# Performance work log

Measured on AMD Instinct MI355X. Metric: run time of the kernel, lower is better.

## Reference

```python
import jax, jax.numpy as jnp
import numpy as np

B, S, D, H = 8, 2048, 1024, 4
HD = D // H


def _layernorm(x, w, b, eps=1e-5):
    mu = jnp.mean(x, axis=-1, keepdims=True)
    var = jnp.mean((x - mu) ** 2, axis=-1, keepdims=True)
    return (x - mu) * jax.lax.rsqrt(var + eps) * w + b


def setup_inputs() -> dict:
    key = jax.random.key(0)
    ks = jax.random.split(key, 10)
    s = 1.0 / np.sqrt(D)
    return {
        "text_representation": jax.random.normal(ks[0], (B, S, D), jnp.float32),
        "image_representation": jax.random.normal(ks[1], (B, S, D), jnp.float32),
        "ln_t_w": jnp.ones((D,), jnp.float32),
        "ln_t_b": jnp.zeros((D,), jnp.float32),
        "ln_i_w": jnp.ones((D,), jnp.float32),
        "ln_i_b": jnp.zeros((D,), jnp.float32),
        "Wa": jax.random.uniform(ks[2], (H, HD, D), jnp.float32, -s, s),
        "Wa_b": jax.random.uniform(ks[3], (H, HD), jnp.float32, -s, s),
        "Wq": jax.random.uniform(ks[4], (H, HD, D), jnp.float32, -s, s),
        "Wq_b": jax.random.uniform(ks[5], (H, HD), jnp.float32, -s, s),
        "sim_w": jax.random.uniform(ks[6], (HD, 1), jnp.float32, -1.0, 1.0),
        "sim_b": jax.random.uniform(ks[7], (HD,), jnp.float32, -1.0, 1.0),
        "fc_w": jax.random.uniform(ks[8], (1, H * HD), jnp.float32, -s, s),
        "fc_b": jax.random.uniform(ks[9], (1,), jnp.float32, -s, s),
    }


def reference(text_representation, image_representation, ln_t_w, ln_t_b,
              ln_i_w, ln_i_b, Wa, Wa_b, Wq, Wq_b, sim_w, sim_b, fc_w, fc_b):
    eps_cos = 1e-6
    text_rep = _layernorm(text_representation, ln_t_w, ln_t_b)   # [B,S,D]
    image_rep = _layernorm(image_representation, ln_i_w, ln_i_b)  # [B,S,D]
    # cosine similarity along last dim (torch-style norm clamping)
    tn = jnp.maximum(jnp.linalg.norm(text_rep, axis=-1), eps_cos)
    im = jnp.maximum(jnp.linalg.norm(image_rep, axis=-1), eps_cos)
    per_pos_sim = jnp.sum(text_rep * image_rep, axis=-1) / (tn * im)  # [B,S]
    global_sim = jnp.mean(per_pos_sim, axis=1, keepdims=True)          # [B,1]
    text_global = jnp.mean(text_rep, axis=1)    # [B,D]
    image_global = jnp.mean(image_rep, axis=1)  # [B,D]
    gate_a = jnp.einsum('bd,hkd->bhk', text_global, Wa) + Wa_b    # [B,H,HD]
    gate_q = jnp.einsum('bd,hkd->bhk', image_global, Wq) + Wq_b   # [B,H,HD]
    sim_feat = global_sim * sim_w[:, 0] + sim_b                   # [B,HD]
    gates = jax.nn.relu(gate_a + gate_q + sim_feat[:, None, :])   # [B,H,HD]
    combined = gates.reshape(gates.shape[0], H * HD)              # [B,H*HD]
    final_gate = jax.nn.sigmoid(combined @ fc_w.T + fc_b)         # [B,1]
    g = final_gate[:, :, None]                                    # [B,1,1]
    return g * text_rep + (1.0 - g) * image_rep
```

## Files before the change

kernel.cpp:

```cpp
#include <hip/hip_runtime.h>
#include <math.h>

#define BB 8
#define SS 2048
#define DD 1024
#define HH 4
#define HDD 256
#define NROW (BB*SS)
#define G 8
#define NSLICE (NROW/G)

#define OFF_MU_T 0
#define OFF_RS_T NROW
#define OFF_MU_I (2*NROW)
#define OFF_RS_I (3*NROW)
#define OFF_PT   (4*NROW)
#define OFF_PI   (OFF_PT + NSLICE*DD)
#define OFF_PS   (OFF_PI + NSLICE*DD)
#define OFF_TG   (OFF_PS + NSLICE)
#define OFF_IG   (OFF_TG + BB*DD)
#define OFF_SIM  (OFF_IG + BB*DD)
#define OFF_LOGIT (OFF_SIM + BB)

__device__ __forceinline__ float wred(float v) {
#pragma unroll
  for (int m = 32; m > 0; m >>= 1) v += __shfl_xor(v, m, 64);
  return v;
}

__device__ __forceinline__ float hsum(const float4 v) { return v.x+v.y+v.z+v.w; }
__device__ __forceinline__ float hsq(const float4 v)  { return v.x*v.x+v.y*v.y+v.z*v.z+v.w*v.w; }
__device__ __forceinline__ float hdot(const float4 a, const float4 b) {
  return a.x*b.x + a.y*b.y + a.z*b.z + a.w*b.w;
}

__global__ __launch_bounds__(256) void k1_stats(
    const float* __restrict__ text, const float* __restrict__ image,
    const float* __restrict__ wt, const float* __restrict__ bt,
    const float* __restrict__ wi, const float* __restrict__ bi,
    float* __restrict__ ws)
{
  const int g    = blockIdx.x;
  const int tid  = threadIdx.x;
  const int lane = tid & 63;
  const int wv   = tid >> 6;
  const int d0   = tid << 2;
  const int row0 = g * G;

  __shared__ float red1[4][8];
  __shared__ float red2[4][6];

  const float4 wt4 = *(const float4*)(wt + d0);
  const float4 bt4 = *(const float4*)(bt + d0);
  const float4 wi4 = *(const float4*)(wi + d0);
  const float4 bi4 = *(const float4*)(bi + d0);

  float4 tga = make_float4(0.f,0.f,0.f,0.f);
  float4 iga = make_float4(0.f,0.f,0.f,0.f);
  float sim_loc = 0.f;

  for (int r = 0; r < G; r += 2) {
    const size_t base0 = (size_t)(row0 + r) * DD + d0;
    const size_t base1 = base0 + DD;
    const float4 t0 = *(const float4*)(text  + base0);
    const float4 i0 = *(const float4*)(image + base0);
    const float4 t1 = *(const float4*)(text  + base1);
    const float4 i1 = *(const float4*)(image + base1);

    float a0 = hsum(t0), a1 = hsq(t0), a2 = hsum(i0), a3 = hsq(i0);
    float a4 = hsum(t1), a5 = hsq(t1), a6 = hsum(i1), a7 = hsq(i1);
    a0 = wred(a0); a1 = wred(a1); a2 = wred(a2); a3 = wred(a3);
    a4 = wred(a4); a5 = wred(a5); a6 = wred(a6); a7 = wred(a7);
    if (lane == 0) {
      red1[wv][0]=a0; red1[wv][1]=a1; red1[wv][2]=a2; red1[wv][3]=a3;
      red1[wv][4]=a4; red1[wv][5]=a5; red1[wv][6]=a6; red1[wv][7]=a7;
    }
    __syncthreads();
    float s[8];
#pragma unroll
    for (int q = 0; q < 8; ++q) s[q] = red1[0][q]+red1[1][q]+red1[2][q]+red1[3][q];
    const float invD = 1.f/DD;
    const float mt0 = s[0]*invD, rt0 = rsqrtf(s[1]*invD - mt0*mt0 + 1e-5f);
    const float mi0 = s[2]*invD, ri0 = rsqrtf(s[3]*invD - mi0*mi0 + 1e-5f);
    const float mt1 = s[4]*invD, rt1 = rsqrtf(s[5]*invD - mt1*mt1 + 1e-5f);
    const float mi1 = s[6]*invD, ri1 = rsqrtf(s[7]*invD - mi1*mi1 + 1e-5f);
    if (tid == 0) {
      const int row = row0 + r;
      ws[OFF_MU_T+row]=mt0;   ws[OFF_RS_T+row]=rt0;
      ws[OFF_MU_I+row]=mi0;   ws[OFF_RS_I+row]=ri0;
      ws[OFF_MU_T+row+1]=mt1; ws[OFF_RS_T+row+1]=rt1;
      ws[OFF_MU_I+row+1]=mi1; ws[OFF_RS_I+row+1]=ri1;
    }
    float4 tn0, in0, tn1, in1;
    tn0.x = (t0.x-mt0)*rt0*wt4.x + bt4.x;  tn0.y = (t0.y-mt0)*rt0*wt4.y + bt4.y;
    tn0.z = (t0.z-mt0)*rt0*wt4.z + bt4.z;  tn0.w = (t0.w-mt0)*rt0*wt4.w + bt4.w;
    in0.x = (i0.x-mi0)*ri0*wi4.x + bi4.x;  in0.y = (i0.y-mi0)*ri0*wi4.y + bi4.y;
    in0.z = (i0.z-mi0)*ri0*wi4.z + bi4.z;  in0.w = (i0.w-mi0)*ri0*wi4.w + bi4.w;
    tn1.x = (t1.x-mt1)*rt1*wt4.x + bt4.x;  tn1.y = (t1.y-mt1)*rt1*wt4.y + bt4.y;
    tn1.z = (t1.z-mt1)*rt1*wt4.z + bt4.z;  tn1.w = (t1.w-mt1)*rt1*wt4.w + bt4.w;
    in1.x = (i1.x-mi1)*ri1*wi4.x + bi4.x;  in1.y = (i1.y-mi1)*ri1*wi4.y + bi4.y;
    in1.z = (i1.z-mi1)*ri1*wi4.z + bi4.z;  in1.w = (i1.w-mi1)*ri1*wi4.w + bi4.w;

    tga.x += tn0.x + tn1.x; tga.y += tn0.y + tn1.y;
    tga.z += tn0.z + tn1.z; tga.w += tn0.w + tn1.w;
    iga.x += in0.x + in1.x; iga.y += in0.y + in1.y;
    iga.z += in0.z + in1.z; iga.w += in0.w + in1.w;

    float b0 = hdot(tn0,in0), b1 = hsq(tn0), b2 = hsq(in0);
    float b3 = hdot(tn1,in1), b4 = hsq(tn1), b5 = hsq(in1);
    b0 = wred(b0); b1 = wred(b1); b2 = wred(b2);
    b3 = wred(b3); b4 = wred(b4); b5 = wred(b5);
    if (lane == 0) {
      red2[wv][0]=b0; red2[wv][1]=b1; red2[wv][2]=b2;
      red2[wv][3]=b3; red2[wv][4]=b4; red2[wv][5]=b5;
    }
    __syncthreads();
    if (tid == 0) {
      float u[6];
#pragma unroll
      for (int q = 0; q < 6; ++q) u[q] = red2[0][q]+red2[1][q]+red2[2][q]+red2[3][q];
      sim_loc += u[0] / (fmaxf(sqrtf(u[1]),1e-6f) * fmaxf(sqrtf(u[2]),1e-6f));
      sim_loc += u[3] / (fmaxf(sqrtf(u[4]),1e-6f) * fmaxf(sqrtf(u[5]),1e-6f));
    }
  }
  *(float4*)(ws + OFF_PT + (size_t)g*DD + d0) = tga;
  *(float4*)(ws + OFF_PI + (size_t)g*DD + d0) = iga;
  if (tid == 0) ws[OFF_PS + g] = sim_loc;
}

__global__ __launch_bounds__(256) void kR_reduce(float* __restrict__ ws)
{
  const int tid = threadIdx.x;
  if (blockIdx.x < 256) {
    const int b   = blockIdx.x >> 5;
    const int ch  = blockIdx.x & 31;
    const int cl  = tid & 31;
    const int sg  = tid >> 5;
    const int col = ch*32 + cl;
    const float* pt = ws + OFF_PT + (size_t)(b*256 + sg*32)*DD + col;
    const float* pi = ws + OFF_PI + (size_t)(b*256 + sg*32)*DD + col;
    float at = 0.f, ai = 0.f;
#pragma unroll 4
    for (int k = 0; k < 32; ++k) {
      at += pt[(size_t)k*DD];
      ai += pi[(size_t)k*DD];
    }
    __shared__ float sred[2][8][32];
    sred[0][sg][cl] = at;
    sred[1][sg][cl] = ai;
    __syncthreads();
    if (tid < 32) {
      float v = 0.f;
#pragma unroll
      for (int q = 0; q < 8; ++q) v += sred[0][q][tid];
      ws[OFF_TG + b*DD + ch*32 + tid] = v;
    } else if (tid < 64) {
      const int c = tid - 32;
      float v = 0.f;
#pragma unroll
      for (int q = 0; q < 8; ++q) v += sred[1][q][c];
      ws[OFF_IG + b*DD + ch*32 + c] = v;
    }
  } else {
    __shared__ float sred[256];
    const int b = tid >> 5, j = tid & 31;
    float a = 0.f;
#pragma unroll
    for (int k = 0; k < 8; ++k) a += ws[OFF_PS + b*256 + j*8 + k];
    sred[tid] = a;
    __syncthreads();
    if (j == 0) {
      float s = 0.f;
#pragma unroll
      for (int m = 0; m < 32; ++m) s += sred[b*32 + m];
      ws[OFF_SIM + b] = s;
    }
    if (tid < BB) ws[OFF_LOGIT + tid] = 0.f;
  }
}

__global__ __launch_bounds__(256) void k2_gates(
    const float* __restrict__ Wa, const float* __restrict__ Wab,
    const float* __restrict__ Wq, const float* __restrict__ Wqb,
    const float* __restrict__ simw, const float* __restrict__ simb,
    const float* __restrict__ fcw, float* __restrict__ ws)
{
  const int tid  = threadIdx.x;
  const int lane = tid & 63;
  const int wv   = tid >> 6;
  const int r0   = blockIdx.x * 4;
  const int d0   = tid << 2;

  __shared__ float red[4][4][BB];

  for (int rr = 0; rr < 4; ++rr) {
    const int r = r0 + rr;
    const float4 a4 = *(const float4*)(Wa + (size_t)r*DD + d0);
    const float4 q4 = *(const float4*)(Wq + (size_t)r*DD + d0);
    float acc[BB];
#pragma unroll
    for (int b = 0; b < BB; ++b) {
      const float4 t = *(const float4*)(ws + OFF_TG + b*DD + d0);
      const float4 i = *(const float4*)(ws + OFF_IG + b*DD + d0);
      acc[b] = hdot(a4, t) + hdot(q4, i);
    }
#pragma unroll
    for (int b = 0; b < BB; ++b) {
      acc[b] = wred(acc[b]);
      if (lane == 0) red[rr][wv][b] = acc[b];
    }
  }
  __syncthreads();
  if (tid < BB) {
    const int b = tid;
    const float inv = 1.f/SS;
    const float gs = ws[OFF_SIM + b] * inv;
    float part = 0.f;
#pragma unroll
    for (int rr = 0; rr < 4; ++rr) {
      const int r = r0 + rr;
      const int k = r & 255;
      const float v = (red[rr][0][b] + red[rr][1][b] + red[rr][2][b] + red[rr][3][b]) * inv;
      float gate = v + Wab[r] + Wqb[r] + gs*simw[k] + simb[k];
      gate = fmaxf(gate, 0.f);
      part += gate * fcw[r];
    }
    atomicAdd(&ws[OFF_LOGIT + b], part);
  }
}

__global__ __launch_bounds__(256) void k3_blend(
    const float* __restrict__ text, const float* __restrict__ image,
    const float* __restrict__ wt, const float* __restrict__ bt,
    const float* __restrict__ wi, const float* __restrict__ bi,
    const float* __restrict__ fcb,
    const float* __restrict__ ws, float* __restrict__ out)
{
  const int r0 = blockIdx.x * 4;
  const int b  = r0 >> 11;
  const int d0 = threadIdx.x << 2;

  float4 t[4], im[4];
#pragma unroll
  for (int r = 0; r < 4; ++r) {
    t[r]  = *(const float4*)(text  + (size_t)(r0+r)*DD + d0);
    im[r] = *(const float4*)(image + (size_t)(r0+r)*DD + d0);
  }
  const float4 wt4 = *(const float4*)(wt + d0);
  const float4 bt4 = *(const float4*)(bt + d0);
  const float4 wi4 = *(const float4*)(wi + d0);
  const float4 bi4 = *(const float4*)(bi + d0);

  const float g  = 1.f / (1.f + expf(-(ws[OFF_LOGIT+b] + fcb[0])));
  const float gi = 1.f - g;

#pragma unroll
  for (int r = 0; r < 4; ++r) {
    const float mt = ws[OFF_MU_T+r0+r], rt = ws[OFF_RS_T+r0+r];
    const float mi = ws[OFF_MU_I+r0+r], ri = ws[OFF_RS_I+r0+r];
    const float gt = g*rt, gii = gi*ri;
    float4 o;
    o.x = gt*(t[r].x-mt)*wt4.x + g*bt4.x + gii*(im[r].x-mi)*wi4.x + gi*bi4.x;
    o.y = gt*(t[r].y-mt)*wt4.y + g*bt4.y + gii*(im[r].y-mi)*wi4.y + gi*bi4.y;
    o.z = gt*(t[r].z-mt)*wt4.z + g*bt4.z + gii*(im[r].z-mi)*wi4.z + gi*bi4.z;
    o.w = gt*(t[r].w-mt)*wt4.w + g*bt4.w + gii*(im[r].w-mi)*wi4.w + gi*bi4.w;
    *(float4*)(out + (size_t)(r0+r)*DD + d0) = o;
  }
}

extern "C" void kernel_launch(void* const* d_in, const int* in_sizes, int n_in,
                              void* d_out, int out_size, void* d_ws, size_t ws_size,
                              hipStream_t stream)
{
  const float* text   = (const float*)d_in[0];
  const float* image  = (const float*)d_in[1];
  const float* ln_t_w = (const float*)d_in[2];
  const float* ln_t_b = (const float*)d_in[3];
  const float* ln_i_w = (const float*)d_in[4];
  const float* ln_i_b = (const float*)d_in[5];
  const float* Wa     = (const float*)d_in[6];
  const float* Wab    = (const float*)d_in[7];
  const float* Wq     = (const float*)d_in[8];
  const float* Wqb    = (const float*)d_in[9];
  const float* simw   = (const float*)d_in[10];
  const float* simb   = (const float*)d_in[11];
  const float* fcw    = (const float*)d_in[12];
  const float* fcb    = (const float*)d_in[13];
  float* ws  = (float*)d_ws;
  float* out = (float*)d_out;

  k1_stats<<<NSLICE, 256, 0, stream>>>(text, image, ln_t_w, ln_t_b, ln_i_w, ln_i_b, ws);
  kR_reduce<<<257, 256, 0, stream>>>(ws);
  k2_gates<<<HH*HDD/4, 256, 0, stream>>>(Wa, Wab, Wq, Wqb, simw, simb, fcw, ws);
  k3_blend<<<NROW/4, 256, 0, stream>>>(text, image, ln_t_w, ln_t_b, ln_i_w, ln_i_b, fcb, ws, out);
}
```

Before: 241.6 us.

## Fuse all four stages into one cooperative kernel with grid-wide syncs

Replaces the four separate launches with one cooperative kernel of 512 blocks that uses grid.sync between the stats, reduction, gate and blend phases. Each wave now owns whole rows, so row statistics come from wave shuffles instead of block barriers. The per-row mean and rstd are kept in shared memory for the blend phase instead of going through the workspace. This removes launch gaps and workspace traffic, at the cost of three grid-wide barriers and a second read of text/image that relies on cache residency. If the cooperative launch fails it falls back to the old four-kernel path.

```diff
diff --git a/kernel.cpp b/kernel.cpp
--- a/kernel.cpp
+++ b/kernel.cpp
@@ -1,5 +1,8 @@
 #include <hip/hip_runtime.h>
+#include <hip/hip_cooperative_groups.h>
 #include <math.h>
+
+namespace cg = cooperative_groups;
 
 #define BB 8
 #define SS 2048
@@ -7,31 +10,260 @@
 #define HH 4
 #define HDD 256
 #define NROW (BB*SS)
-#define G 8
-#define NSLICE (NROW/G)
-
-#define OFF_MU_T 0
-#define OFF_RS_T NROW
-#define OFF_MU_I (2*NROW)
-#define OFF_RS_I (3*NROW)
-#define OFF_PT   (4*NROW)
-#define OFF_PI   (OFF_PT + NSLICE*DD)
-#define OFF_PS   (OFF_PI + NSLICE*DD)
-#define OFF_TG   (OFF_PS + NSLICE)
-#define OFF_IG   (OFF_TG + BB*DD)
-#define OFF_SIM  (OFF_IG + BB*DD)
+
+#define GG 32
+#define NBLK (NROW/GG)
+#define NSL  (NBLK*4)
+
+#define OFF_PT 0
+#define OFF_PI (OFF_PT + NSL*DD)
+#define OFF_PS (OFF_PI + NSL*DD)
+#define OFF_TG (OFF_PS + NSL)
+#define OFF_IG (OFF_TG + BB*DD)
+#define OFF_SIM (OFF_IG + BB*DD)
 #define OFF_LOGIT (OFF_SIM + BB)
+
+#define GF 8
+#define NSLF (NROW/GF)
+#define F_MU_T 0
+#define F_RS_T NROW
+#define F_MU_I (2*NROW)
+#define F_RS_I (3*NROW)
+#define F_PT   (4*NROW)
+#define F_PI   (F_PT + NSLF*DD)
+#define F_PS   (F_PI + NSLF*DD)
+#define F_TG   (F_PS + NSLF)
+#define F_IG   (F_TG + BB*DD)
+#define F_SIM  (F_IG + BB*DD)
+#define F_LOGIT (F_SIM + BB)
 
 __device__ __forceinline__ float wred(float v) {
 #pragma unroll
   for (int m = 32; m > 0; m >>= 1) v += __shfl_xor(v, m, 64);
   return v;
 }
-
 __device__ __forceinline__ float hsum(const float4 v) { return v.x+v.y+v.z+v.w; }
 __device__ __forceinline__ float hsq(const float4 v)  { return v.x*v.x+v.y*v.y+v.z*v.z+v.w*v.w; }
 __device__ __forceinline__ float hdot(const float4 a, const float4 b) {
   return a.x*b.x + a.y*b.y + a.z*b.z + a.w*b.w;
+}
+
+__global__ __launch_bounds__(256, 2) void fused(
+    const float* __restrict__ text, const float* __restrict__ image,
+    const float* __restrict__ wt, const float* __restrict__ bt,
+    const float* __restrict__ wi, const float* __restrict__ bi,
+    const float* __restrict__ Wa, const float* __restrict__ Wab,
+    const float* __restrict__ Wq, const float* __restrict__ Wqb,
+    const float* __restrict__ simw, const float* __restrict__ simb,
+    const float* __restrict__ fcw, const float* __restrict__ fcb,
+    float* __restrict__ ws, float* __restrict__ out)
+{
+  cg::grid_group grid = cg::this_grid();
+  const int blk  = blockIdx.x;
+  const int tid  = threadIdx.x;
+  const int lane = tid & 63;
+  const int wv   = tid >> 6;
+  const int row0 = blk * GG;
+
+  __shared__ float smu_t[GG], srs_t[GG], smu_i[GG], srs_i[GG];
+  __shared__ float sred[2][8][32];
+  __shared__ float red3[4][4][BB];
+
+  {
+    const int cb = lane << 2;
+    float4 Wt[4], Bt[4], Wi4[4], Bi4[4];
+#pragma unroll
+    for (int j = 0; j < 4; ++j) {
+      Wt[j]  = *(const float4*)(wt + j*256 + cb);
+      Bt[j]  = *(const float4*)(bt + j*256 + cb);
+      Wi4[j] = *(const float4*)(wi + j*256 + cb);
+      Bi4[j] = *(const float4*)(bi + j*256 + cb);
+    }
+    float4 tga[4], iga[4];
+#pragma unroll
+    for (int j = 0; j < 4; ++j) {
+      tga[j] = make_float4(0.f,0.f,0.f,0.f);
+      iga[j] = make_float4(0.f,0.f,0.f,0.f);
+    }
+    float sim_loc = 0.f;
+    const float invD = 1.f/DD;
+    const int rbase = row0 + wv*8;
+
+#pragma unroll 1
+    for (int r = 0; r < 8; ++r) {
+      const float* trow = text  + (size_t)(rbase + r)*DD + cb;
+      const float* irow = image + (size_t)(rbase + r)*DD + cb;
+      float4 t[4], im[4];
+#pragma unroll
+      for (int j = 0; j < 4; ++j) t[j]  = *(const float4*)(trow + j*256);
+#pragma unroll
+      for (int j = 0; j < 4; ++j) im[j] = *(const float4*)(irow + j*256);
+
+      float st=0.f, qt=0.f, si=0.f, qi=0.f;
+#pragma unroll
+      for (int j = 0; j < 4; ++j) {
+        st += hsum(t[j]);  qt += hsq(t[j]);
+        si += hsum(im[j]); qi += hsq(im[j]);
+      }
+      st = wred(st); qt = wred(qt); si = wred(si); qi = wred(qi);
+      const float mt = st*invD, rt = rsqrtf(qt*invD - mt*mt + 1e-5f);
+      const float mi = si*invD, ri = rsqrtf(qi*invD - mi*mi + 1e-5f);
+      if (lane == 0) {
+        smu_t[wv*8+r]=mt; srs_t[wv*8+r]=rt;
+        smu_i[wv*8+r]=mi; srs_i[wv*8+r]=ri;
+      }
+
+      float dot=0.f, nt=0.f, ni=0.f;
+#pragma unroll
+      for (int j = 0; j < 4; ++j) {
+        float4 tn, iv;
+        tn.x = (t[j].x-mt)*rt*Wt[j].x + Bt[j].x;
+        tn.y = (t[j].y-mt)*rt*Wt[j].y + Bt[j].y;
+        tn.z = (t[j].z-mt)*rt*Wt[j].z + Bt[j].z;
+        tn.w = (t[j].w-mt)*rt*Wt[j].w + Bt[j].w;
+        iv.x = (im[j].x-mi)*ri*Wi4[j].x + Bi4[j].x;
+        iv.y = (im[j].y-mi)*ri*Wi4[j].y + Bi4[j].y;
+        iv.z = (im[j].z-mi)*ri*Wi4[j].z + Bi4[j].z;
+        iv.w = (im[j].w-mi)*ri*Wi4[j].w + Bi4[j].w;
+        tga[j].x += tn.x; tga[j].y += tn.y; tga[j].z += tn.z; tga[j].w += tn.w;
+        iga[j].x += iv.x; iga[j].y += iv.y; iga[j].z += iv.z; iga[j].w += iv.w;
+        dot += hdot(tn, iv); nt += hsq(tn); ni += hsq(iv);
+      }
+      dot = wred(dot); nt = wred(nt); ni = wred(ni);
+      sim_loc += dot / (fmaxf(sqrtf(nt),1e-6f) * fmaxf(sqrtf(ni),1e-6f));
+    }
+
+    const int slice = blk*4 + wv;
+#pragma unroll
+    for (int j = 0; j < 4; ++j) {
+      *(float4*)(ws + OFF_PT + (size_t)slice*DD + j*256 + cb) = tga[j];
+      *(float4*)(ws + OFF_PI + (size_t)slice*DD + j*256 + cb) = iga[j];
+    }
+    if (lane == 0) ws[OFF_PS + slice] = sim_loc;
+  }
+
+  grid.sync();
+
+  if (blk < 256) {
+    const int b   = blk >> 5;
+    const int ch  = blk & 31;
+    const int cl  = tid & 31;
+    const int sg  = tid >> 5;
+    const int col = ch*32 + cl;
+    const float* pt = ws + OFF_PT + (size_t)(b*256 + sg*32)*DD + col;
+    const float* pi = ws + OFF_PI + (size_t)(b*256 + sg*32)*DD + col;
+    float at = 0.f, ai = 0.f;
+#pragma unroll 4
+    for (int k = 0; k < 32; ++k) {
+      at += pt[(size_t)k*DD];
+      ai += pi[(size_t)k*DD];
+    }
+    sred[0][sg][cl] = at;
+    sred[1][sg][cl] = ai;
+    __syncthreads();
+    if (tid < 32) {
+      float v = 0.f;
+#pragma unroll
+      for (int q = 0; q < 8; ++q) v += sred[0][q][tid];
+      ws[OFF_TG + b*DD + ch*32 + tid] = v;
+    } else if (tid < 64) {
+      const int c = tid - 32;
+      float v = 0.f;
+#pragma unroll
+      for (int q = 0; q < 8; ++q) v += sred[1][q][c];
+      ws[OFF_IG + b*DD + ch*32 + c] = v;
+    }
+  } else if (blk == 256) {
+    float* sflat = (float*)sred;
+    const int b = tid >> 5, j = tid & 31;
+    float a = 0.f;
+#pragma unroll
+    for (int k = 0; k < 8; ++k) a += ws[OFF_PS + b*256 + j*8 + k];
+    sflat[tid] = a;
+    __syncthreads();
+    if (j == 0) {
+      float ssum = 0.f;
+#pragma unroll
+      for (int m = 0; m < 32; ++m) ssum += sflat[b*32 + m];
+      ws[OFF_SIM + b] = ssum;
+    }
+    if (tid < BB) ws[OFF_LOGIT + tid] = 0.f;
+  }
+
+  grid.sync();
+
+  if (blk < 256) {
+    const int d0 = tid << 2;
+    const int r0 = blk * 4;
+    for (int rr = 0; rr < 4; ++rr) {
+      const int r = r0 + rr;
+      const float4 a4 = *(const float4*)(Wa + (size_t)r*DD + d0);
+      const float4 q4 = *(const float4*)(Wq + (size_t)r*DD + d0);
+      float acc[BB];
+#pragma unroll
+      for (int b = 0; b < BB; ++b) {
+        const float4 t = *(const float4*)(ws + OFF_TG + b*DD + d0);
+        const float4 i = *(const float4*)(ws + OFF_IG + b*DD + d0);
+        acc[b] = hdot(a4, t) + hdot(q4, i);
+      }
+#pragma unroll
+      for (int b = 0; b < BB; ++b) {
+        acc[b] = wred(acc[b]);
+        if (lane == 0) red3[rr][wv][b] = acc[b];
+      }
+    }
+    __syncthreads();
+    if (tid < BB) {
+      const int b = tid;
+      const float inv = 1.f/SS;
+      const float gs = ws[OFF_SIM + b] * inv;
+      float part = 0.f;
+#pragma unroll
+      for (int rr = 0; rr < 4; ++rr) {
+        const int r = r0 + rr;
+        const int k = r & 255;
+        const float v = (red3[rr][0][b] + red3[rr][1][b] + red3[rr][2][b] + red3[rr][3][b]) * inv;
+        float gate = v + Wab[r] + Wqb[r] + gs*simw[k] + simb[k];
+        gate = fmaxf(gate, 0.f);
+        part += gate * fcw[r];
+      }
+      atomicAdd(&ws[OFF_LOGIT + b], part);
+    }
+  }
+
+  grid.sync();
+
+  {
+    const int d0 = tid << 2;
+    const float4 wt4 = *(const float4*)(wt + d0);
+    const float4 bt4 = *(const float4*)(bt + d0);
+    const float4 wi4 = *(const float4*)(wi + d0);
+    const float4 bi4 = *(const float4*)(bi + d0);
+    const int b = row0 >> 11;
+    const float g  = 1.f / (1.f + expf(-(ws[OFF_LOGIT + b] + fcb[0])));
+    const float gi = 1.f - g;
+#pragma unroll 1
+    for (int rr = 0; rr < GG; rr += 4) {
+      float4 t[4], im[4];
+#pragma unroll
+      for (int r = 0; r < 4; ++r) {
+        t[r]  = *(const float4*)(text  + (size_t)(row0+rr+r)*DD + d0);
+        im[r] = *(const float4*)(image + (size_t)(row0+rr+r)*DD + d0);
+      }
+#pragma unroll
+      for (int r = 0; r < 4; ++r) {
+        const float mt = smu_t[rr+r], rt = srs_t[rr+r];
+        const float mi = smu_i[rr+r], ri = srs_i[rr+r];
+        const float gt = g*rt, gii = gi*ri;
+        float4 o;
+        o.x = gt*(t[r].x-mt)*wt4.x + g*bt4.x + gii*(im[r].x-mi)*wi4.x + gi*bi4.x;
+        o.y = gt*(t[r].y-mt)*wt4.y + g*bt4.y + gii*(im[r].y-mi)*wi4.y + gi*bi4.y;
+        o.z = gt*(t[r].z-mt)*wt4.z + g*bt4.z + gii*(im[r].z-mi)*wi4.z + gi*bi4.z;
+        o.w = gt*(t[r].w-mt)*wt4.w + g*bt4.w + gii*(im[r].w-mi)*wi4.w + gi*bi4.w;
+        *(float4*)(out + (size_t)(row0+rr+r)*DD + d0) = o;
+      }
+    }
+  }
 }
 
 __global__ __launch_bounds__(256) void k1_stats(
@@ -45,7 +277,7 @@
   const int lane = tid & 63;
   const int wv   = tid >> 6;
   const int d0   = tid << 2;
-  const int row0 = g * G;
+  const int row0 = g * GF;
 
   __shared__ float red1[4][8];
   __shared__ float red2[4][6];
@@ -59,7 +291,7 @@
   float4 iga = make_float4(0.f,0.f,0.f,0.f);
   float sim_loc = 0.f;
 
-  for (int r = 0; r < G; r += 2) {
+  for (int r = 0; r < GF; r += 2) {
     const size_t base0 = (size_t)(row0 + r) * DD + d0;
     const size_t base1 = base0 + DD;
     const float4 t0 = *(const float4*)(text  + base0);
@@ -86,10 +318,10 @@
     const float mi1 = s[6]*invD, ri1 = rsqrtf(s[7]*invD - mi1*mi1 + 1e-5f);
     if (tid == 0) {
       const int row = row0 + r;
-      ws[OFF_MU_T+row]=mt0;   ws[OFF_RS_T+row]=rt0;
-      ws[OFF_MU_I+row]=mi0;   ws[OFF_RS_I+row]=ri0;
-      ws[OFF_MU_T+row+1]=mt1; ws[OFF_RS_T+row+1]=rt1;
-      ws[OFF_MU_I+row+1]=mi1; ws[OFF_RS_I+row+1]=ri1;
+      ws[F_MU_T+row]=mt0;   ws[F_RS_T+row]=rt0;
+      ws[F_MU_I+row]=mi0;   ws[F_RS_I+row]=ri0;
+      ws[F_MU_T+row+1]=mt1; ws[F_RS_T+row+1]=rt1;
+      ws[F_MU_I+row+1]=mi1; ws[F_RS_I+row+1]=ri1;
     }
     float4 tn0, in0, tn1, in1;
     tn0.x = (t0.x-mt0)*rt0*wt4.x + bt4.x;  tn0.y = (t0.y-mt0)*rt0*wt4.y + bt4.y;
@@ -123,9 +355,9 @@
       sim_loc += u[3] / (fmaxf(sqrtf(u[4]),1e-6f) * fmaxf(sqrtf(u[5]),1e-6f));
     }
   }
-  *(float4*)(ws + OFF_PT + (size_t)g*DD + d0) = tga;
-  *(float4*)(ws + OFF_PI + (size_t)g*DD + d0) = iga;
-  if (tid == 0) ws[OFF_PS + g] = sim_loc;
+  *(float4*)(ws + F_PT + (size_t)g*DD + d0) = tga;
+  *(float4*)(ws + F_PI + (size_t)g*DD + d0) = iga;
+  if (tid == 0) ws[F_PS + g] = sim_loc;
 }
 
 __global__ __launch_bounds__(256) void kR_reduce(float* __restrict__ ws)
@@ -137,8 +369,8 @@
     const int cl  = tid & 31;
     const int sg  = tid >> 5;
     const int col = ch*32 + cl;
-    const float* pt = ws + OFF_PT + (size_t)(b*256 + sg*32)*DD + col;
-    const float* pi = ws + OFF_PI + (size_t)(b*256 + sg*32)*DD + col;
+    const float* pt = ws + F_PT + (size_t)(b*256 + sg*32)*DD + col;
+    const float* pi = ws + F_PI + (size_t)(b*256 + sg*32)*DD + col;
     float at = 0.f, ai = 0.f;
 #pragma unroll 4
     for (int k = 0; k < 32; ++k) {
@@ -153,29 +385,29 @@
       float v = 0.f;
 #pragma unroll
       for (int q = 0; q < 8; ++q) v += sred[0][q][tid];
-      ws[OFF_TG + b*DD + ch*32 + tid] = v;
+      ws[F_TG + b*DD + ch*32 + tid] = v;
     } else if (tid < 64) {
       const int c = tid - 32;
       float v = 0.f;
 #pragma unroll
       for (int q = 0; q < 8; ++q) v += sred[1][q][c];
-      ws[OFF_IG + b*DD + ch*32 + c] = v;
+      ws[F_IG + b*DD + ch*32 + c] = v;
     }
   } else {
     __shared__ float sred[256];
     const int b = tid >> 5, j = tid & 31;
     float a = 0.f;
 #pragma unroll
-    for (int k = 0; k < 8; ++k) a += ws[OFF_PS + b*256 + j*8 + k];
+    for (int k = 0; k < 8; ++k) a += ws[F_PS + b*256 + j*8 + k];
     sred[tid] = a;
     __syncthreads();
     if (j == 0) {
       float s = 0.f;
 #pragma unroll
       for (int m = 0; m < 32; ++m) s += sred[b*32 + m];
-      ws[OFF_SIM + b] = s;
-    }
-    if (tid < BB) ws[OFF_LOGIT + tid] = 0.f;
+      ws[F_SIM + b] = s;
+    }
+    if (tid < BB) ws[F_LOGIT + tid] = 0.f;
   }
 }
 
@@ -200,8 +432,8 @@
     float acc[BB];
 #pragma unroll
     for (int b = 0; b < BB; ++b) {
-      const float4 t = *(const float4*)(ws + OFF_TG + b*DD + d0);
-      const float4 i = *(const float4*)(ws + OFF_IG + b*DD + d0);
+      const float4 t = *(const float4*)(ws + F_TG + b*DD + d0);
+      const float4 i = *(const float4*)(ws + F_IG + b*DD + d0);
       acc[b] = hdot(a4, t) + hdot(q4, i);
     }
 #pragma unroll
@@ -214,7 +446,7 @@
   if (tid < BB) {
     const int b = tid;
     const float inv = 1.f/SS;
-    const float gs = ws[OFF_SIM + b] * inv;
+    const float gs = ws[F_SIM + b] * inv;
     float part = 0.f;
 #pragma unroll
     for (int rr = 0; rr < 4; ++rr) {
@@ -225,7 +457,7 @@
       gate = fmaxf(gate, 0.f);
       part += gate * fcw[r];
     }
-    atomicAdd(&ws[OFF_LOGIT + b], part);
+    atomicAdd(&ws[F_LOGIT + b], part);
   }
 }
 
@@ -251,13 +483,13 @@
   const float4 wi4 = *(const float4*)(wi + d0);
   const float4 bi4 = *(const float4*)(bi + d0);
 
-  const float g  = 1.f / (1.f + expf(-(ws[OFF_LOGIT+b] + fcb[0])));
+  const float g  = 1.f / (1.f + expf(-(ws[F_LOGIT+b] + fcb[0])));
   const float gi = 1.f - g;
 
 #pragma unroll
   for (int r = 0; r < 4; ++r) {
-    const float mt = ws[OFF_MU_T+r0+r], rt = ws[OFF_RS_T+r0+r];
-    const float mi = ws[OFF_MU_I+r0+r], ri = ws[OFF_RS_I+r0+r];
+    const float mt = ws[F_MU_T+r0+r], rt = ws[F_RS_T+r0+r];
+    const float mi = ws[F_MU_I+r0+r], ri = ws[F_RS_I+r0+r];
     const float gt = g*rt, gii = gi*ri;
     float4 o;
     o.x = gt*(t[r].x-mt)*wt4.x + g*bt4.x + gii*(im[r].x-mi)*wi4.x + gi*bi4.x;
@@ -289,7 +521,21 @@
   float* ws  = (float*)d_ws;
   float* out = (float*)d_out;
 
-  k1_stats<<<NSLICE, 256, 0, stream>>>(text, image, ln_t_w, ln_t_b, ln_i_w, ln_i_b, ws);
+  static int use_coop = -1;
+  if (use_coop != 0) {
+    void* args[16] = {
+      (void*)&text, (void*)&image, (void*)&ln_t_w, (void*)&ln_t_b,
+      (void*)&ln_i_w, (void*)&ln_i_b, (void*)&Wa, (void*)&Wab,
+      (void*)&Wq, (void*)&Wqb, (void*)&simw, (void*)&simb,
+      (void*)&fcw, (void*)&fcb, (void*)&ws, (void*)&out
+    };
+    hipError_t e = hipLaunchCooperativeKernel((void*)fused, dim3(NBLK), dim3(256),
+                                              args, 0, stream);
+    if (e == hipSuccess) { use_coop = 1; return; }
+    use_coop = 0;
+  }
+
+  k1_stats<<<NSLF, 256, 0, stream>>>(text, image, ln_t_w, ln_t_b, ln_i_w, ln_i_b, ws);
   kR_reduce<<<257, 256, 0, stream>>>(ws);
   k2_gates<<<HH*HDD/4, 256, 0, stream>>>(Wa, Wab, Wq, Wqb, simw, simb, fcw, ws);
   k3_blend<<<NROW/4, 256, 0, stream>>>(text, image, ln_t_w, ln_t_b, ln_i_w, ln_i_b, fcb, ws, out);
```

New measurement: 244.0 us. Within noise of the previous version (+1.0%).
